# Kernel optimization log

Hardware: AMD Instinct MI355X
Metric: run time of the kernel (lower is better)

## Reference

```python
import jax, jax.numpy as jnp
import numpy as np

N_NODES = 100000
N_EDGES = 1600000
N_FEAT = 512
N_HID = 256
N_CLASS = 40


def setup_inputs() -> dict:
    key = jax.random.key(0)
    ks = jax.random.split(key, 6)
    features = jax.random.normal(ks[0], (N_NODES, N_FEAT), dtype=jnp.float32)
    edge_index = jax.random.randint(ks[1], (2, N_EDGES), 0, N_NODES, dtype=jnp.int32)
    edge_weight = jax.random.uniform(ks[2], (N_EDGES,), dtype=jnp.float32)
    # xavier_uniform with gain=1.414 (as in reset_parameters)
    g = 1.414
    lim1 = g * np.sqrt(6.0 / (N_FEAT + N_HID))
    lim2 = g * np.sqrt(6.0 / (N_HID + N_CLASS))
    W1 = jax.random.uniform(ks[3], (N_FEAT, N_HID), minval=-lim1, maxval=lim1, dtype=jnp.float32)
    W2 = jax.random.uniform(ks[4], (N_HID, N_CLASS), minval=-lim2, maxval=lim2, dtype=jnp.float32)
    b1 = jnp.zeros((N_HID,), dtype=jnp.float32)
    b2 = jnp.zeros((N_CLASS,), dtype=jnp.float32)
    return {"features": features, "edge_index": edge_index, "edge_weight": edge_weight,
            "W1": W1, "b1": b1, "W2": W2, "b2": b2}


def _spmm(edge_index, edge_weight, x, n):
    # out[r] = sum over edges e with row[e]==r of w[e] * x[col[e]]
    row, col = edge_index[0], edge_index[1]
    msgs = edge_weight[:, None] * x[col]  # [E, D]
    return jax.ops.segment_sum(msgs, row, num_segments=n)


def reference(features, edge_index, edge_weight, W1, b1, W2, b2):
    n = features.shape[0]
    # Layer 1: linear -> spmm -> relu (dropout is identity in eval mode)
    h = features @ W1 + b1
    h = jax.nn.relu(_spmm(edge_index, edge_weight, h, n))
    # Layer 2: linear -> spmm -> log_softmax
    h = h @ W2 + b2
    h = _spmm(edge_index, edge_weight, h, n)
    return jax.nn.log_softmax(h, axis=1)
```

## Files before the change

### kernel.cpp

```cpp
#include <hip/hip_runtime.h>
#include <stdint.h>

#define N_NODES 100000
#define N_EDGES 1600000
#define N_FEAT 512
#define N_HID 256
#define N_CLASS 40
#define H2S 48

typedef float f32x4 __attribute__((ext_vector_type(4)));
typedef __bf16 bf16x8 __attribute__((ext_vector_type(8)));
typedef unsigned short u16x4 __attribute__((ext_vector_type(4)));
typedef unsigned short u16x8 __attribute__((ext_vector_type(8)));

__device__ __forceinline__ unsigned short f2bf(float f) {
  unsigned int u = __float_as_uint(f);
  unsigned int r = (u + 0x7FFFu + ((u >> 16) & 1u)) >> 16;
  return (unsigned short)r;
}
__device__ __forceinline__ float bf2f(unsigned short s) {
  return __uint_as_float(((unsigned int)s) << 16);
}
__device__ __forceinline__ float pk_w(unsigned int p) {
  return __uint_as_float((p >> 17) << 16);
}
__device__ __forceinline__ int pk_c(unsigned int p) { return (int)(p & 0x1FFFFu); }

#define HIST_BLOCKS 1563
#define W1T_BLOCKS  512
#define W2T_BLOCKS  48
__global__ __launch_bounds__(256) void k_pre(const float* __restrict__ W1,
                                             const float* __restrict__ W2,
                                             const int* __restrict__ ei,
                                             unsigned short* __restrict__ W1t,
                                             unsigned short* __restrict__ W2t,
                                             int* __restrict__ cnt,
                                             int* __restrict__ rank) {
  const int bid = blockIdx.x, tid = threadIdx.x;
  if (bid < HIST_BLOCKS) {
    #pragma unroll
    for (int k = 0; k < 4; ++k) {
      int e = bid * 1024 + k * 256 + tid;
      if (e < N_EDGES) rank[e] = atomicAdd(&cnt[ei[e]], 1);
    }
  } else if (bid < HIST_BLOCKS + W1T_BLOCKS) {
    int gid = (bid - HIST_BLOCKS) * 256 + tid;
    int n = gid >> 9, k = gid & 511;
    W1t[gid] = f2bf(W1[(long)k * N_HID + n]);
  } else {
    int gid = (bid - HIST_BLOCKS - W1T_BLOCKS) * 256 + tid;
    int n = gid >> 8, k = gid & 255;
    W2t[gid] = (n < N_CLASS) ? f2bf(W2[(long)k * N_CLASS + n]) : (unsigned short)0;
  }
}

__global__ __launch_bounds__(1024) void k_scan_a(const int* __restrict__ cnt,
                                                 int* __restrict__ rp,
                                                 int* __restrict__ bsum) {
  __shared__ int sm[1024];
  const int tid = threadIdx.x;
  const int i = blockIdx.x * 1024 + tid;
  int v = (i < N_NODES) ? cnt[i] : 0;
  sm[tid] = v;
  __syncthreads();
  #pragma unroll
  for (int d = 1; d < 1024; d <<= 1) {
    int t = (tid >= d) ? sm[tid - d] : 0;
    __syncthreads();
    sm[tid] += t;
    __syncthreads();
  }
  if (i < N_NODES) rp[i] = sm[tid] - v;
  if (tid == 1023) bsum[blockIdx.x] = sm[1023];
}

__global__ __launch_bounds__(128) void k_scan_b(const int* __restrict__ bsum,
                                                int* __restrict__ boffs,
                                                int* __restrict__ rp) {
  __shared__ int sm[128];
  const int tid = threadIdx.x;
  const int nb = (N_NODES + 1023) >> 10;
  int v = (tid < nb) ? bsum[tid] : 0;
  sm[tid] = v;
  __syncthreads();
  #pragma unroll
  for (int d = 1; d < 128; d <<= 1) {
    int t = (tid >= d) ? sm[tid - d] : 0;
    __syncthreads();
    sm[tid] += t;
    __syncthreads();
  }
  boffs[tid] = sm[tid] - v;
  if (tid == 127) rp[N_NODES] = sm[127];
}

__global__ void k_scan_c(int* __restrict__ rp, const int* __restrict__ boffs) {
  int i = blockIdx.x * 256 + threadIdx.x;
  if (i >= N_NODES) return;
  rp[i] += boffs[i >> 10];
}

__global__ __launch_bounds__(512) void k_scatter(const int* __restrict__ ei,
                                                 const float* __restrict__ ew,
                                                 const int* __restrict__ rank,
                                                 const int* __restrict__ rp,
                                                 unsigned int* __restrict__ cwp) {
  const int t = threadIdx.x;
  #pragma unroll
  for (int k = 0; k < 4; ++k) {
    int e = blockIdx.x * 2048 + k * 512 + t;
    if (e < N_EDGES) {
      int r = ei[e];
      int pos = rp[r] + rank[e];
      unsigned int w15 = (unsigned int)f2bf(ew[e]);
      cwp[pos] = (w15 << 17) | (unsigned int)ei[N_EDGES + e];
    }
  }
}

__global__ __launch_bounds__(1024) void k_gemm1(const float* __restrict__ X,
                                                const unsigned short* __restrict__ W1t,
                                                const float* __restrict__ b1,
                                                unsigned short* __restrict__ H1) {
  __shared__ __align__(16) unsigned short Bs[128 * 512];
  const int t = threadIdx.x;
  const int pair = blockIdx.x >> 1, panel = blockIdx.x & 1;
  const long rb = (long)pair * 800;
  const int n0 = panel * 128;

  {
    const int col = t >> 3, seg = t & 7;
    const unsigned short* src = W1t + (long)(n0 + col) * N_FEAT;
    #pragma unroll
    for (int j = 0; j < 8; ++j) {
      int slot = seg * 8 + j;
      int ps = slot ^ (col & 7);
      *(u16x8*)&Bs[col * 512 + ps * 8] = *(const u16x8*)(src + slot * 8);
    }
  }
  __syncthreads();

  const int lane = t & 63;
  const int wid = t >> 6;
  const int lr = lane & 15;
  const int lkg = lane >> 4;

  for (int c = wid; c < 50; c += 16) {
    const long row0 = rb + c * 16;
    const float* ap = X + (row0 + lr) * N_FEAT + lkg * 8;
    f32x4 acc[8] = {};

    #pragma unroll 2
    for (int k0 = 0; k0 < N_FEAT; k0 += 32) {
      f32x4 xa = *(const f32x4*)(ap + k0);
      f32x4 xb = *(const f32x4*)(ap + k0 + 4);
      bf16x8 av;
      av[0] = (__bf16)xa[0]; av[1] = (__bf16)xa[1];
      av[2] = (__bf16)xa[2]; av[3] = (__bf16)xa[3];
      av[4] = (__bf16)xb[0]; av[5] = (__bf16)xb[1];
      av[6] = (__bf16)xb[2]; av[7] = (__bf16)xb[3];
      const int slot = (k0 >> 3) + lkg;
      const int ps = slot ^ (lr & 7);
      #pragma unroll
      for (int nt = 0; nt < 8; ++nt) {
        bf16x8 bv = *(const bf16x8*)&Bs[(nt * 16 + lr) * 512 + ps * 8];
        acc[nt] = __builtin_amdgcn_mfma_f32_16x16x32_bf16(av, bv, acc[nt], 0, 0, 0);
      }
    }

    #pragma unroll
    for (int nt = 0; nt < 8; ++nt) {
      int colg = n0 + nt * 16 + lr;
      float bias = b1[colg];
      #pragma unroll
      for (int i = 0; i < 4; ++i) {
        long row = row0 + lkg * 4 + i;
        H1[row * N_HID + colg] = f2bf(acc[nt][i] + bias);
      }
    }
  }
}

__global__ __launch_bounds__(256) void k_spmm1(const int* __restrict__ row_ptr,
                                               const unsigned int* __restrict__ cwp,
                                               const unsigned short* __restrict__ H1,
                                               unsigned short* __restrict__ H1r) {
  int r = blockIdx.x * 4 + (threadIdx.x >> 6);
  int lane = threadIdx.x & 63;
  if (r >= N_NODES) return;
  int s = row_ptr[r], e = row_ptr[r + 1];
  float a0 = 0.f, a1 = 0.f, a2 = 0.f, a3 = 0.f;
  const unsigned short* Hb = H1 + lane * 4;
  int i = s;
  for (; i + 8 <= e; i += 8) {
    uint4 ca = *(const uint4*)(cwp + i);
    uint4 cb = *(const uint4*)(cwp + i + 4);
    u16x4 h0 = *(const u16x4*)(Hb + (long)pk_c(ca.x) * N_HID);
    u16x4 h1 = *(const u16x4*)(Hb + (long)pk_c(ca.y) * N_HID);
    u16x4 h2 = *(const u16x4*)(Hb + (long)pk_c(ca.z) * N_HID);
    u16x4 h3 = *(const u16x4*)(Hb + (long)pk_c(ca.w) * N_HID);
    u16x4 h4 = *(const u16x4*)(Hb + (long)pk_c(cb.x) * N_HID);
    u16x4 h5 = *(const u16x4*)(Hb + (long)pk_c(cb.y) * N_HID);
    u16x4 h6 = *(const u16x4*)(Hb + (long)pk_c(cb.z) * N_HID);
    u16x4 h7 = *(const u16x4*)(Hb + (long)pk_c(cb.w) * N_HID);
    float w0 = pk_w(ca.x), w1 = pk_w(ca.y), w2 = pk_w(ca.z), w3 = pk_w(ca.w);
    float w4 = pk_w(cb.x), w5 = pk_w(cb.y), w6 = pk_w(cb.z), w7 = pk_w(cb.w);
    a0 += w0 * bf2f(h0[0]); a1 += w0 * bf2f(h0[1]); a2 += w0 * bf2f(h0[2]); a3 += w0 * bf2f(h0[3]);
    a0 += w1 * bf2f(h1[0]); a1 += w1 * bf2f(h1[1]); a2 += w1 * bf2f(h1[2]); a3 += w1 * bf2f(h1[3]);
    a0 += w2 * bf2f(h2[0]); a1 += w2 * bf2f(h2[1]); a2 += w2 * bf2f(h2[2]); a3 += w2 * bf2f(h2[3]);
    a0 += w3 * bf2f(h3[0]); a1 += w3 * bf2f(h3[1]); a2 += w3 * bf2f(h3[2]); a3 += w3 * bf2f(h3[3]);
    a0 += w4 * bf2f(h4[0]); a1 += w4 * bf2f(h4[1]); a2 += w4 * bf2f(h4[2]); a3 += w4 * bf2f(h4[3]);
    a0 += w5 * bf2f(h5[0]); a1 += w5 * bf2f(h5[1]); a2 += w5 * bf2f(h5[2]); a3 += w5 * bf2f(h5[3]);
    a0 += w6 * bf2f(h6[0]); a1 += w6 * bf2f(h6[1]); a2 += w6 * bf2f(h6[2]); a3 += w6 * bf2f(h6[3]);
    a0 += w7 * bf2f(h7[0]); a1 += w7 * bf2f(h7[1]); a2 += w7 * bf2f(h7[2]); a3 += w7 * bf2f(h7[3]);
  }
  for (; i < e; ++i) {
    unsigned int p = cwp[i];
    float w = pk_w(p);
    u16x4 hv = *(const u16x4*)(Hb + (long)pk_c(p) * N_HID);
    a0 += w * bf2f(hv[0]);
    a1 += w * bf2f(hv[1]);
    a2 += w * bf2f(hv[2]);
    a3 += w * bf2f(hv[3]);
  }
  u16x4 o;
  o[0] = f2bf(fmaxf(a0, 0.f));
  o[1] = f2bf(fmaxf(a1, 0.f));
  o[2] = f2bf(fmaxf(a2, 0.f));
  o[3] = f2bf(fmaxf(a3, 0.f));
  *(u16x4*)(H1r + (long)r * N_HID + lane * 4) = o;
}

__global__ __launch_bounds__(256) void k_gemm2(const unsigned short* __restrict__ H1r,
                                               const unsigned short* __restrict__ W2t,
                                               const float* __restrict__ b2,
                                               float* __restrict__ H2) {
  const int t = threadIdx.x;
  const int lane = t & 63;
  const int wid = t >> 6;
  const long m0 = (long)blockIdx.x * 128;
  const int lr = lane & 15;
  const int lk = (lane >> 4) * 8;

  const unsigned short* Ab[2];
  #pragma unroll
  for (int mt = 0; mt < 2; ++mt) {
    long r = m0 + wid * 32 + mt * 16 + lr;
    if (r >= N_NODES) r = N_NODES - 1;
    Ab[mt] = H1r + r * N_HID + lk;
  }
  const unsigned short* Bb[3];
  #pragma unroll
  for (int nt = 0; nt < 3; ++nt)
    Bb[nt] = W2t + (long)(nt * 16 + lr) * N_HID + lk;

  f32x4 acc[2][3] = {};
  #pragma unroll
  for (int k0 = 0; k0 < N_HID; k0 += 32) {
    bf16x8 av[2], bvv[3];
    #pragma unroll
    for (int mt = 0; mt < 2; ++mt) av[mt] = *(const bf16x8*)(Ab[mt] + k0);
    #pragma unroll
    for (int nt = 0; nt < 3; ++nt) bvv[nt] = *(const bf16x8*)(Bb[nt] + k0);
    #pragma unroll
    for (int mt = 0; mt < 2; ++mt)
      #pragma unroll
      for (int nt = 0; nt < 3; ++nt)
        acc[mt][nt] = __builtin_amdgcn_mfma_f32_16x16x32_bf16(av[mt], bvv[nt], acc[mt][nt], 0, 0, 0);
  }

  #pragma unroll
  for (int nt = 0; nt < 3; ++nt) {
    int col = nt * 16 + lr;
    if (col < N_CLASS) {
      float bias = b2[col];
      #pragma unroll
      for (int mt = 0; mt < 2; ++mt) {
        #pragma unroll
        for (int i = 0; i < 4; ++i) {
          long row = m0 + wid * 32 + mt * 16 + (lane >> 4) * 4 + i;
          if (row < N_NODES) H2[row * H2S + col] = acc[mt][nt][i] + bias;
        }
      }
    }
  }
}

__global__ __launch_bounds__(256) void k_spmm2_lsm(const int* __restrict__ row_ptr,
                                                   const unsigned int* __restrict__ cwp,
                                                   const float* __restrict__ H2,
                                                   float* __restrict__ out) {
  int r = blockIdx.x * 4 + (threadIdx.x >> 6);
  int lane = threadIdx.x & 63;
  if (r >= N_NODES) return;
  int s = row_ptr[r], e = row_ptr[r + 1];
  float acc = 0.f;
  const bool act = lane < N_CLASS;
  int i = s;
  for (; i + 8 <= e; i += 8) {
    uint4 ca = *(const uint4*)(cwp + i);
    uint4 cb = *(const uint4*)(cwp + i + 4);
    float h0 = 0.f, h1 = 0.f, h2 = 0.f, h3 = 0.f, h4 = 0.f, h5 = 0.f, h6 = 0.f, h7 = 0.f;
    if (act) {
      h0 = H2[(long)pk_c(ca.x) * H2S + lane];
      h1 = H2[(long)pk_c(ca.y) * H2S + lane];
      h2 = H2[(long)pk_c(ca.z) * H2S + lane];
      h3 = H2[(long)pk_c(ca.w) * H2S + lane];
      h4 = H2[(long)pk_c(cb.x) * H2S + lane];
      h5 = H2[(long)pk_c(cb.y) * H2S + lane];
      h6 = H2[(long)pk_c(cb.z) * H2S + lane];
      h7 = H2[(long)pk_c(cb.w) * H2S + lane];
    }
    acc += pk_w(ca.x) * h0;
    acc += pk_w(ca.y) * h1;
    acc += pk_w(ca.z) * h2;
    acc += pk_w(ca.w) * h3;
    acc += pk_w(cb.x) * h4;
    acc += pk_w(cb.y) * h5;
    acc += pk_w(cb.z) * h6;
    acc += pk_w(cb.w) * h7;
  }
  for (; i < e; ++i) {
    unsigned int p = cwp[i];
    if (act) acc += pk_w(p) * H2[(long)pk_c(p) * H2S + lane];
  }
  float v = act ? acc : -INFINITY;
  float m = v;
  #pragma unroll
  for (int d = 32; d > 0; d >>= 1) m = fmaxf(m, __shfl_xor(m, d));
  float ex = act ? __expf(v - m) : 0.f;
  float ssum = ex;
  #pragma unroll
  for (int d = 32; d > 0; d >>= 1) ssum += __shfl_xor(ssum, d);
  float ls = __logf(ssum);
  if (act) out[(long)r * N_CLASS + lane] = v - m - ls;
}

extern "C" void kernel_launch(void* const* d_in, const int* in_sizes, int n_in,
                              void* d_out, int out_size, void* d_ws, size_t ws_size,
                              hipStream_t stream) {
  (void)in_sizes; (void)n_in; (void)out_size; (void)ws_size;
  const float* X  = (const float*)d_in[0];
  const int*   EI = (const int*)d_in[1];
  const float* EW = (const float*)d_in[2];
  const float* W1 = (const float*)d_in[3];
  const float* b1 = (const float*)d_in[4];
  const float* W2 = (const float*)d_in[5];
  const float* b2 = (const float*)d_in[6];
  float* out = (float*)d_out;

  char* p = (char*)d_ws;
  auto take = [&](size_t bytes) {
    char* r = p;
    p += (bytes + 511) & ~(size_t)511;
    return r;
  };
  unsigned short* W1t   = (unsigned short*)take((size_t)N_HID * N_FEAT * 2);
  unsigned short* W2t   = (unsigned short*)take((size_t)48 * N_HID * 2);
  int*            cnt   = (int*)take((size_t)N_NODES * 4);
  int*            rp    = (int*)take((size_t)(N_NODES + 1) * 4);
  int*            bsum  = (int*)take((size_t)128 * 4);
  int*            boffs = (int*)take((size_t)128 * 4);
  int*            rank  = (int*)take((size_t)N_EDGES * 4);
  unsigned int*   cwp   = (unsigned int*)take((size_t)N_EDGES * 4);
  unsigned short* H1    = (unsigned short*)take((size_t)N_NODES * N_HID * 2);
  unsigned short* H1r   = (unsigned short*)take((size_t)N_NODES * N_HID * 2);
  float*          H2    = (float*)take((size_t)N_NODES * H2S * 4);

  const int NB_SCAN = (N_NODES + 1023) / 1024;

  hipMemsetAsync(cnt, 0, (size_t)N_NODES * 4, stream);
  k_pre<<<HIST_BLOCKS + W1T_BLOCKS + W2T_BLOCKS, 256, 0, stream>>>(W1, W2, EI, W1t, W2t, cnt, rank);
  k_scan_a<<<NB_SCAN, 1024, 0, stream>>>(cnt, rp, bsum);
  k_scan_b<<<1, 128, 0, stream>>>(bsum, boffs, rp);
  k_scan_c<<<(N_NODES + 255) / 256, 256, 0, stream>>>(rp, boffs);
  k_scatter<<<(N_EDGES + 2047) / 2048, 512, 0, stream>>>(EI, EW, rank, rp, cwp);
  k_gemm1<<<250, 1024, 0, stream>>>(X, W1t, b1, H1);
  k_spmm1<<<(N_NODES + 3) / 4, 256, 0, stream>>>(rp, cwp, H1, H1r);
  k_gemm2<<<(N_NODES + 127) / 128, 256, 0, stream>>>(H1r, W2t, b2, H2);
  k_spmm2_lsm<<<(N_NODES + 3) / 4, 256, 0, stream>>>(rp, cwp, H2, out);
}
```

Measured before the change: 427.0 us.

## Store layer-2 logits in bf16, deepen spmm1 unroll, replace memset with zero kernel

Three separate changes. The layer-2 projection H2 is now stored as bf16 with a 64-element row stride instead of fp32 with stride 48, which halves the bytes gathered per edge in the second spmm. The first spmm's inner loop is unrolled to 16 edges, with a new 4-edge tail loop, so more independent gathers are in flight. The hipMemsetAsync on the count array is replaced by a small zeroing kernel to cut API overhead. Rounding the logits to bf16 before aggregation adds some error to the output.

```diff
diff --git a/kernel.cpp b/kernel.cpp
--- a/kernel.cpp
+++ b/kernel.cpp
@@ -6,7 +6,7 @@
 #define N_FEAT 512
 #define N_HID 256
 #define N_CLASS 40
-#define H2S 48
+#define H2SB 64
 
 typedef float f32x4 __attribute__((ext_vector_type(4)));
 typedef __bf16 bf16x8 __attribute__((ext_vector_type(8)));
@@ -25,6 +25,11 @@
   return __uint_as_float((p >> 17) << 16);
 }
 __device__ __forceinline__ int pk_c(unsigned int p) { return (int)(p & 0x1FFFFu); }
+
+__global__ __launch_bounds__(1024) void k_zero(int* __restrict__ cnt) {
+  int i = blockIdx.x * 1024 + threadIdx.x;
+  if (i < N_NODES) cnt[i] = 0;
+}
 
 #define HIST_BLOCKS 1563
 #define W1T_BLOCKS  512
@@ -192,27 +197,41 @@
   float a0 = 0.f, a1 = 0.f, a2 = 0.f, a3 = 0.f;
   const unsigned short* Hb = H1 + lane * 4;
   int i = s;
-  for (; i + 8 <= e; i += 8) {
-    uint4 ca = *(const uint4*)(cwp + i);
-    uint4 cb = *(const uint4*)(cwp + i + 4);
-    u16x4 h0 = *(const u16x4*)(Hb + (long)pk_c(ca.x) * N_HID);
-    u16x4 h1 = *(const u16x4*)(Hb + (long)pk_c(ca.y) * N_HID);
-    u16x4 h2 = *(const u16x4*)(Hb + (long)pk_c(ca.z) * N_HID);
-    u16x4 h3 = *(const u16x4*)(Hb + (long)pk_c(ca.w) * N_HID);
-    u16x4 h4 = *(const u16x4*)(Hb + (long)pk_c(cb.x) * N_HID);
-    u16x4 h5 = *(const u16x4*)(Hb + (long)pk_c(cb.y) * N_HID);
-    u16x4 h6 = *(const u16x4*)(Hb + (long)pk_c(cb.z) * N_HID);
-    u16x4 h7 = *(const u16x4*)(Hb + (long)pk_c(cb.w) * N_HID);
-    float w0 = pk_w(ca.x), w1 = pk_w(ca.y), w2 = pk_w(ca.z), w3 = pk_w(ca.w);
-    float w4 = pk_w(cb.x), w5 = pk_w(cb.y), w6 = pk_w(cb.z), w7 = pk_w(cb.w);
-    a0 += w0 * bf2f(h0[0]); a1 += w0 * bf2f(h0[1]); a2 += w0 * bf2f(h0[2]); a3 += w0 * bf2f(h0[3]);
-    a0 += w1 * bf2f(h1[0]); a1 += w1 * bf2f(h1[1]); a2 += w1 * bf2f(h1[2]); a3 += w1 * bf2f(h1[3]);
-    a0 += w2 * bf2f(h2[0]); a1 += w2 * bf2f(h2[1]); a2 += w2 * bf2f(h2[2]); a3 += w2 * bf2f(h2[3]);
-    a0 += w3 * bf2f(h3[0]); a1 += w3 * bf2f(h3[1]); a2 += w3 * bf2f(h3[2]); a3 += w3 * bf2f(h3[3]);
-    a0 += w4 * bf2f(h4[0]); a1 += w4 * bf2f(h4[1]); a2 += w4 * bf2f(h4[2]); a3 += w4 * bf2f(h4[3]);
-    a0 += w5 * bf2f(h5[0]); a1 += w5 * bf2f(h5[1]); a2 += w5 * bf2f(h5[2]); a3 += w5 * bf2f(h5[3]);
-    a0 += w6 * bf2f(h6[0]); a1 += w6 * bf2f(h6[1]); a2 += w6 * bf2f(h6[2]); a3 += w6 * bf2f(h6[3]);
-    a0 += w7 * bf2f(h7[0]); a1 += w7 * bf2f(h7[1]); a2 += w7 * bf2f(h7[2]); a3 += w7 * bf2f(h7[3]);
+  for (; i + 16 <= e; i += 16) {
+    uint4 q0 = *(const uint4*)(cwp + i);
+    uint4 q1 = *(const uint4*)(cwp + i + 4);
+    uint4 q2 = *(const uint4*)(cwp + i + 8);
+    uint4 q3 = *(const uint4*)(cwp + i + 12);
+    unsigned int cc[16] = {q0.x, q0.y, q0.z, q0.w, q1.x, q1.y, q1.z, q1.w,
+                           q2.x, q2.y, q2.z, q2.w, q3.x, q3.y, q3.z, q3.w};
+    u16x4 h[16];
+    #pragma unroll
+    for (int j = 0; j < 16; ++j)
+      h[j] = *(const u16x4*)(Hb + (long)pk_c(cc[j]) * N_HID);
+    #pragma unroll
+    for (int j = 0; j < 16; ++j) {
+      float w = pk_w(cc[j]);
+      a0 += w * bf2f(h[j][0]);
+      a1 += w * bf2f(h[j][1]);
+      a2 += w * bf2f(h[j][2]);
+      a3 += w * bf2f(h[j][3]);
+    }
+  }
+  for (; i + 4 <= e; i += 4) {
+    uint4 q = *(const uint4*)(cwp + i);
+    unsigned int cc[4] = {q.x, q.y, q.z, q.w};
+    u16x4 h[4];
+    #pragma unroll
+    for (int j = 0; j < 4; ++j)
+      h[j] = *(const u16x4*)(Hb + (long)pk_c(cc[j]) * N_HID);
+    #pragma unroll
+    for (int j = 0; j < 4; ++j) {
+      float w = pk_w(cc[j]);
+      a0 += w * bf2f(h[j][0]);
+      a1 += w * bf2f(h[j][1]);
+      a2 += w * bf2f(h[j][2]);
+      a3 += w * bf2f(h[j][3]);
+    }
   }
   for (; i < e; ++i) {
     unsigned int p = cwp[i];
@@ -234,7 +253,7 @@
 __global__ __launch_bounds__(256) void k_gemm2(const unsigned short* __restrict__ H1r,
                                                const unsigned short* __restrict__ W2t,
                                                const float* __restrict__ b2,
-                                               float* __restrict__ H2) {
+                                               unsigned short* __restrict__ H2) {
   const int t = threadIdx.x;
   const int lane = t & 63;
   const int wid = t >> 6;
@@ -279,7 +298,7 @@
         #pragma unroll
         for (int i = 0; i < 4; ++i) {
           long row = m0 + wid * 32 + mt * 16 + (lane >> 4) * 4 + i;
-          if (row < N_NODES) H2[row * H2S + col] = acc[mt][nt][i] + bias;
+          if (row < N_NODES) H2[row * H2SB + col] = f2bf(acc[mt][nt][i] + bias);
         }
       }
     }
@@ -288,7 +307,7 @@
 
 __global__ __launch_bounds__(256) void k_spmm2_lsm(const int* __restrict__ row_ptr,
                                                    const unsigned int* __restrict__ cwp,
-                                                   const float* __restrict__ H2,
+                                                   const unsigned short* __restrict__ H2,
                                                    float* __restrict__ out) {
   int r = blockIdx.x * 4 + (threadIdx.x >> 6);
   int lane = threadIdx.x & 63;
@@ -298,31 +317,19 @@
   const bool act = lane < N_CLASS;
   int i = s;
   for (; i + 8 <= e; i += 8) {
-    uint4 ca = *(const uint4*)(cwp + i);
-    uint4 cb = *(const uint4*)(cwp + i + 4);
-    float h0 = 0.f, h1 = 0.f, h2 = 0.f, h3 = 0.f, h4 = 0.f, h5 = 0.f, h6 = 0.f, h7 = 0.f;
-    if (act) {
-      h0 = H2[(long)pk_c(ca.x) * H2S + lane];
-      h1 = H2[(long)pk_c(ca.y) * H2S + lane];
-      h2 = H2[(long)pk_c(ca.z) * H2S + lane];
-      h3 = H2[(long)pk_c(ca.w) * H2S + lane];
-      h4 = H2[(long)pk_c(cb.x) * H2S + lane];
-      h5 = H2[(long)pk_c(cb.y) * H2S + lane];
-      h6 = H2[(long)pk_c(cb.z) * H2S + lane];
-      h7 = H2[(long)pk_c(cb.w) * H2S + lane];
-    }
-    acc += pk_w(ca.x) * h0;
-    acc += pk_w(ca.y) * h1;
-    acc += pk_w(ca.z) * h2;
-    acc += pk_w(ca.w) * h3;
-    acc += pk_w(cb.x) * h4;
-    acc += pk_w(cb.y) * h5;
-    acc += pk_w(cb.z) * h6;
-    acc += pk_w(cb.w) * h7;
+    uint4 q0 = *(const uint4*)(cwp + i);
+    uint4 q1 = *(const uint4*)(cwp + i + 4);
+    unsigned int cc[8] = {q0.x, q0.y, q0.z, q0.w, q1.x, q1.y, q1.z, q1.w};
+    float h[8];
+    #pragma unroll
+    for (int j = 0; j < 8; ++j)
+      h[j] = act ? bf2f(H2[(long)pk_c(cc[j]) * H2SB + lane]) : 0.f;
+    #pragma unroll
+    for (int j = 0; j < 8; ++j) acc += pk_w(cc[j]) * h[j];
   }
   for (; i < e; ++i) {
     unsigned int p = cwp[i];
-    if (act) acc += pk_w(p) * H2[(long)pk_c(p) * H2S + lane];
+    if (act) acc += pk_w(p) * bf2f(H2[(long)pk_c(p) * H2SB + lane]);
   }
   float v = act ? acc : -INFINITY;
   float m = v;
@@ -365,11 +372,11 @@
   unsigned int*   cwp   = (unsigned int*)take((size_t)N_EDGES * 4);
   unsigned short* H1    = (unsigned short*)take((size_t)N_NODES * N_HID * 2);
   unsigned short* H1r   = (unsigned short*)take((size_t)N_NODES * N_HID * 2);
-  float*          H2    = (float*)take((size_t)N_NODES * H2S * 4);
+  unsigned short* H2    = (unsigned short*)take((size_t)N_NODES * H2SB * 2);
 
   const int NB_SCAN = (N_NODES + 1023) / 1024;
 
-  hipMemsetAsync(cnt, 0, (size_t)N_NODES * 4, stream);
+  k_zero<<<NB_SCAN, 1024, 0, stream>>>(cnt);
   k_pre<<<HIST_BLOCKS + W1T_BLOCKS + W2T_BLOCKS, 256, 0, stream>>>(W1, W2, EI, W1t, W2t, cnt, rank);
   k_scan_a<<<NB_SCAN, 1024, 0, stream>>>(cnt, rp, bsum);
   k_scan_b<<<1, 128, 0, stream>>>(bsum, boffs, rp);
```

Result: slower. 466.3 us (+9.2%).
